# Kernel optimization log

Measured on AMD Instinct MI355X. Metric: run time of the kernel, lower is better.

The kernel has to match this reference:

```python
import jax, jax.numpy as jnp
import numpy as np

B, H, W, C = 32, 112, 112, 128
R = 2048  # make_divisible(128*16, 8)

def setup_inputs() -> dict:
    key = jax.random.key(0)
    k1, k2, k3 = jax.random.split(key, 3)
    x = jax.random.normal(k1, (B, H, W, C), dtype=jnp.float32)
    w1 = jax.random.normal(k2, (C, R), dtype=jnp.float32) * (1.0 / np.sqrt(C))
    b1 = jnp.zeros((R,), dtype=jnp.float32)
    w2 = jax.random.normal(k3, (R, C), dtype=jnp.float32) * (1.0 / np.sqrt(R))
    b2 = jnp.zeros((C,), dtype=jnp.float32)
    return {"x": x, "w1": w1, "b1": b1, "w2": w2, "b2": b2}

def reference(x, w1, b1, w2, b2):
    # squeeze: global average pool over H, W -> [B, C]
    s = jnp.mean(x, axis=(1, 2))
    # excite: two 1x1 convs on pooled vector == matmuls
    h = jax.nn.gelu(s @ w1 + b1)          # [B, R], tanh-approx GELU (tfa default)
    g = jax.nn.sigmoid(h @ w2 + b2)       # [B, C]
    # broadcast gate over spatial dims
    return x * g[:, None, None, :]
```

## Files before the change

### kernel.cpp

```cpp
#include <hip/hip_runtime.h>
#include <math.h>

#define B_ 32
#define H_ 112
#define W_ 112
#define C_ 128
#define R_ 2048
#define HW_ (H_ * W_)
#define C4_ (C_ / 4)
#define PB_ 32

typedef float f32x4_t __attribute__((ext_vector_type(4)));

__global__ __launch_bounds__(256) void pool_kernel(const float4* __restrict__ x,
                                                   float4* __restrict__ part) {
    const int b     = blockIdx.x;
    const int pb    = blockIdx.y;
    const int t     = threadIdx.x;
    const int lane4 = t & 31;
    const int prow  = t >> 5;

    const int pixels_per_block = HW_ / PB_;
    const int p0 = pb * pixels_per_block;
    const float4* xb = x + (size_t)b * HW_ * C4_;

    float4 acc = make_float4(0.f, 0.f, 0.f, 0.f);
    for (int p = p0 + prow; p < p0 + pixels_per_block; p += 8) {
        float4 v = xb[(size_t)p * C4_ + lane4];
        acc.x += v.x; acc.y += v.y; acc.z += v.z; acc.w += v.w;
    }

    __shared__ float4 red[256];
    red[t] = acc;
    __syncthreads();
    if (t < 32) {
        float4 a = red[t];
#pragma unroll
        for (int k = 1; k < 8; ++k) {
            float4 v = red[t + 32 * k];
            a.x += v.x; a.y += v.y; a.z += v.z; a.w += v.w;
        }
        part[((size_t)b * PB_ + pb) * C4_ + t] = a;
    }
}

__global__ __launch_bounds__(256) void fc1_kernel(const float4* __restrict__ part,
                                                  const float* __restrict__ w1,
                                                  const float* __restrict__ b1,
                                                  float* __restrict__ h) {
    const int b  = blockIdx.x >> 3;
    const int rb = blockIdx.x & 7;
    const int r  = rb * 256 + threadIdx.x;
    const int t  = threadIdx.x;

    __shared__ float sl[C_];
    if (t < 32) {
        float4 a = make_float4(0.f, 0.f, 0.f, 0.f);
#pragma unroll 8
        for (int k = 0; k < PB_; ++k) {
            float4 v = part[((size_t)b * PB_ + k) * C4_ + t];
            a.x += v.x; a.y += v.y; a.z += v.z; a.w += v.w;
        }
        const float inv = 1.0f / (float)HW_;
        sl[t * 4 + 0] = a.x * inv;
        sl[t * 4 + 1] = a.y * inv;
        sl[t * 4 + 2] = a.z * inv;
        sl[t * 4 + 3] = a.w * inv;
    }
    __syncthreads();

    float acc = b1[r];
#pragma unroll 8
    for (int c = 0; c < C_; ++c)
        acc += sl[c] * w1[(size_t)c * R_ + r];

    const float xv = acc;
    const float tn = tanhf(0.7978845608028654f * (xv + 0.044715f * xv * xv * xv));
    h[(size_t)b * R_ + r] = 0.5f * xv * (1.0f + tn);
}

__global__ __launch_bounds__(256) void fc2_kernel(const float* __restrict__ h,
                                                  const float4* __restrict__ w2,
                                                  const float* __restrict__ b2,
                                                  float4* __restrict__ g) {
    const int b     = blockIdx.x;
    const int t     = threadIdx.x;
    const int c4    = t & 31;
    const int slice = t >> 5;

    __shared__ float hl[R_];
    for (int i = t; i < R_; i += 256) hl[i] = h[(size_t)b * R_ + i];
    __syncthreads();

    float4 acc = make_float4(0.f, 0.f, 0.f, 0.f);
    const int r0 = slice * (R_ / 8);
#pragma unroll 4
    for (int r = r0; r < r0 + R_ / 8; ++r) {
        const float hv = hl[r];
        float4 w = w2[(size_t)r * C4_ + c4];
        acc.x += hv * w.x; acc.y += hv * w.y; acc.z += hv * w.z; acc.w += hv * w.w;
    }

    __shared__ float4 partl[256];
    partl[t] = acc;
    __syncthreads();
    if (t < 32) {
        float4 a = partl[t];
#pragma unroll
        for (int k = 1; k < 8; ++k) {
            float4 v = partl[t + 32 * k];
            a.x += v.x; a.y += v.y; a.z += v.z; a.w += v.w;
        }
        a.x += b2[t * 4 + 0]; a.y += b2[t * 4 + 1];
        a.z += b2[t * 4 + 2]; a.w += b2[t * 4 + 3];
        float4 gv;
        gv.x = 1.0f / (1.0f + expf(-a.x));
        gv.y = 1.0f / (1.0f + expf(-a.y));
        gv.z = 1.0f / (1.0f + expf(-a.z));
        gv.w = 1.0f / (1.0f + expf(-a.w));
        g[(size_t)b * C4_ + t] = gv;
    }
}

__global__ __launch_bounds__(256) void scale_kernel(const float4* __restrict__ x,
                                                    const float4* __restrict__ g,
                                                    float4* __restrict__ out) {
    const int b  = blockIdx.x;
    const int t  = threadIdx.x;
    const int c4 = t & 31;

    const float4 gv = g[(size_t)b * C4_ + c4];
    const size_t base = (size_t)b * HW_ * C4_;
    const int total = HW_ * C4_;
    const int stride = gridDim.y * 256;

    for (int i = blockIdx.y * 256 + t; i < total; i += stride) {
        float4 v = x[base + i];
        f32x4_t o;
        o.x = v.x * gv.x; o.y = v.y * gv.y; o.z = v.z * gv.z; o.w = v.w * gv.w;
        __builtin_nontemporal_store(o, (f32x4_t*)&out[base + i]);
    }
}

extern "C" void kernel_launch(void* const* d_in, const int* in_sizes, int n_in,
                              void* d_out, int out_size, void* d_ws, size_t ws_size,
                              hipStream_t stream) {
    const float* x  = (const float*)d_in[0];
    const float* w1 = (const float*)d_in[1];
    const float* b1 = (const float*)d_in[2];
    const float* w2 = (const float*)d_in[3];
    const float* b2 = (const float*)d_in[4];
    float* out = (float*)d_out;

    float* part = (float*)d_ws;
    float* h    = part + B_ * PB_ * C_;
    float* g    = h + B_ * R_;

    pool_kernel<<<dim3(B_, PB_), 256, 0, stream>>>((const float4*)x, (float4*)part);
    fc1_kernel<<<B_ * 8, 256, 0, stream>>>((const float4*)part, w1, b1, h);
    fc2_kernel<<<B_, 256, 0, stream>>>(h, (const float4*)w2, b2, (float4*)g);
    scale_kernel<<<dim3(B_, 64), 256, 0, stream>>>((const float4*)x, (const float4*)g,
                                                   (float4*)out);
}
```

Baseline: 421.1 us.

## Fuse fc1 and fc2 into one kernel with split-K partials reduced in scale

Merges the two FC kernels into one. Each block computes its 256-wide slice of the GELU hidden vector in shared memory and immediately multiplies it by the matching rows of w2, writing partial gate sums per slice. The scale kernel then reduces the 8 partials, adds the bias and applies the sigmoid before gating x. This removes one kernel launch, the global round-trip for h, and the poorly parallel 32-block fc2 stage, at the cost of redundant partial reduction in every scale block.

```diff
diff --git a/kernel.cpp b/kernel.cpp
--- a/kernel.cpp
+++ b/kernel.cpp
@@ -9,6 +9,7 @@
 #define HW_ (H_ * W_)
 #define C4_ (C_ / 4)
 #define PB_ 32
+#define RB_ 8
 
 typedef float f32x4_t __attribute__((ext_vector_type(4)));
 
@@ -44,16 +45,20 @@
     }
 }
 
-__global__ __launch_bounds__(256) void fc1_kernel(const float4* __restrict__ part,
-                                                  const float* __restrict__ w1,
-                                                  const float* __restrict__ b1,
-                                                  float* __restrict__ h) {
+__global__ __launch_bounds__(256) void fc_kernel(const float4* __restrict__ part,
+                                                 const float* __restrict__ w1,
+                                                 const float* __restrict__ b1,
+                                                 const float4* __restrict__ w2,
+                                                 float4* __restrict__ gpart) {
     const int b  = blockIdx.x >> 3;
     const int rb = blockIdx.x & 7;
-    const int r  = rb * 256 + threadIdx.x;
     const int t  = threadIdx.x;
+    const int r  = rb * 256 + t;
 
-    __shared__ float sl[C_];
+    __shared__ float  sl[C_];
+    __shared__ float  hl[256];
+    __shared__ float4 red[256];
+
     if (t < 32) {
         float4 a = make_float4(0.f, 0.f, 0.f, 0.f);
 #pragma unroll 8
@@ -76,60 +81,55 @@
 
     const float xv = acc;
     const float tn = tanhf(0.7978845608028654f * (xv + 0.044715f * xv * xv * xv));
-    h[(size_t)b * R_ + r] = 0.5f * xv * (1.0f + tn);
-}
-
-__global__ __launch_bounds__(256) void fc2_kernel(const float* __restrict__ h,
-                                                  const float4* __restrict__ w2,
-                                                  const float* __restrict__ b2,
-                                                  float4* __restrict__ g) {
-    const int b     = blockIdx.x;
-    const int t     = threadIdx.x;
-    const int c4    = t & 31;
-    const int slice = t >> 5;
-
-    __shared__ float hl[R_];
-    for (int i = t; i < R_; i += 256) hl[i] = h[(size_t)b * R_ + i];
+    hl[t] = 0.5f * xv * (1.0f + tn);
     __syncthreads();
 
-    float4 acc = make_float4(0.f, 0.f, 0.f, 0.f);
-    const int r0 = slice * (R_ / 8);
-#pragma unroll 4
-    for (int r = r0; r < r0 + R_ / 8; ++r) {
-        const float hv = hl[r];
-        float4 w = w2[(size_t)r * C4_ + c4];
-        acc.x += hv * w.x; acc.y += hv * w.y; acc.z += hv * w.z; acc.w += hv * w.w;
+    const int c4 = t & 31;
+    const int ks = t >> 5;
+    float4 a2 = make_float4(0.f, 0.f, 0.f, 0.f);
+    const int rr0 = ks * 32;
+#pragma unroll 8
+    for (int rr = rr0; rr < rr0 + 32; ++rr) {
+        const float hv = hl[rr];
+        float4 w = w2[(size_t)(rb * 256 + rr) * C4_ + c4];
+        a2.x += hv * w.x; a2.y += hv * w.y; a2.z += hv * w.z; a2.w += hv * w.w;
     }
-
-    __shared__ float4 partl[256];
-    partl[t] = acc;
+    red[t] = a2;
     __syncthreads();
     if (t < 32) {
-        float4 a = partl[t];
+        float4 a = red[t];
 #pragma unroll
         for (int k = 1; k < 8; ++k) {
-            float4 v = partl[t + 32 * k];
+            float4 v = red[t + 32 * k];
             a.x += v.x; a.y += v.y; a.z += v.z; a.w += v.w;
         }
-        a.x += b2[t * 4 + 0]; a.y += b2[t * 4 + 1];
-        a.z += b2[t * 4 + 2]; a.w += b2[t * 4 + 3];
-        float4 gv;
-        gv.x = 1.0f / (1.0f + expf(-a.x));
-        gv.y = 1.0f / (1.0f + expf(-a.y));
-        gv.z = 1.0f / (1.0f + expf(-a.z));
-        gv.w = 1.0f / (1.0f + expf(-a.w));
-        g[(size_t)b * C4_ + t] = gv;
+        gpart[((size_t)b * RB_ + rb) * C4_ + t] = a;
     }
 }
 
 __global__ __launch_bounds__(256) void scale_kernel(const float4* __restrict__ x,
-                                                    const float4* __restrict__ g,
+                                                    const float4* __restrict__ gpart,
+                                                    const float* __restrict__ b2,
                                                     float4* __restrict__ out) {
     const int b  = blockIdx.x;
     const int t  = threadIdx.x;
     const int c4 = t & 31;
 
-    const float4 gv = g[(size_t)b * C4_ + c4];
+    const float4* gp = gpart + (size_t)b * RB_ * C4_;
+    float4 a = gp[c4];
+#pragma unroll
+    for (int k = 1; k < RB_; ++k) {
+        float4 v = gp[(size_t)k * C4_ + c4];
+        a.x += v.x; a.y += v.y; a.z += v.z; a.w += v.w;
+    }
+    a.x += b2[c4 * 4 + 0]; a.y += b2[c4 * 4 + 1];
+    a.z += b2[c4 * 4 + 2]; a.w += b2[c4 * 4 + 3];
+    float4 gv;
+    gv.x = 1.0f / (1.0f + expf(-a.x));
+    gv.y = 1.0f / (1.0f + expf(-a.y));
+    gv.z = 1.0f / (1.0f + expf(-a.z));
+    gv.w = 1.0f / (1.0f + expf(-a.w));
+
     const size_t base = (size_t)b * HW_ * C4_;
     const int total = HW_ * C4_;
     const int stride = gridDim.y * 256;
@@ -152,13 +152,13 @@
     const float* b2 = (const float*)d_in[4];
     float* out = (float*)d_out;
 
-    float* part = (float*)d_ws;
-    float* h    = part + B_ * PB_ * C_;
-    float* g    = h + B_ * R_;
+    float* part  = (float*)d_ws;
+    float* gpart = part + B_ * PB_ * C_;
 
     pool_kernel<<<dim3(B_, PB_), 256, 0, stream>>>((const float4*)x, (float4*)part);
-    fc1_kernel<<<B_ * 8, 256, 0, stream>>>((const float4*)part, w1, b1, h);
-    fc2_kernel<<<B_, 256, 0, stream>>>(h, (const float4*)w2, b2, (float4*)g);
-    scale_kernel<<<dim3(B_, 64), 256, 0, stream>>>((const float4*)x, (const float4*)g,
+    fc_kernel<<<B_ * RB_, 256, 0, stream>>>((const float4*)part, w1, b1,
+                                            (const float4*)w2, (float4*)gpart);
+    scale_kernel<<<dim3(B_, 64), 256, 0, stream>>>((const float4*)x,
+                                                   (const float4*)gpart, b2,
                                                    (float4*)out);
 }
```

Measured after the change: 393.4 us. 6.6% less time.
